# Performance work log

Hardware: AMD Instinct MI355X
Metric: run time of the kernel (lower is better)

The kernel has to match this reference:

```python
import jax, jax.numpy as jnp
import numpy as np

MOD = 26
N = 64  # module init arg n
B = 1024


def _mul_map():
    # A[p, k, v] = 1 where v = p*k mod MOD
    P_, K_ = np.meshgrid(np.arange(MOD), np.arange(MOD), indexing='ij')
    A = np.zeros((MOD, MOD, MOD), dtype=np.float32)
    A[P_, K_, (P_ * K_) % MOD] = 1.0
    return A


def _circ_conv(a, b):
    # circular convolution of length MOD via rfft/irfft, then clamp+normalize
    c = jnp.fft.irfft(jnp.fft.rfft(a, n=MOD) * jnp.fft.rfft(b, n=MOD), n=MOD)
    c = jnp.clip(c, 0.0)
    s = jnp.sum(c, axis=-1, keepdims=True)
    s = jnp.where(s == 0, jnp.ones_like(s), s)
    return c / s


def setup_inputs() -> dict:
    key = jax.random.key(0)
    k1, k2 = jax.random.split(key)
    P = jax.random.randint(k1, (B, N), 0, MOD)
    key_param = jax.random.normal(k2, (N * N, MOD), dtype=jnp.float32) * 0.01
    return {"P": P, "key_param": key_param}


def reference(P, key_param):
    n = N
    key_probs = jax.nn.softmax(key_param, axis=-1).reshape(n, n, MOD)
    A = jnp.asarray(_mul_map())  # [p, k, v]
    P_onehot = jax.nn.one_hot(P, MOD, dtype=jnp.float32)  # [B, n, MOD]
    # torch.tensordot(key_probs, A, dims=([2],[1])) -> [l, i, p, c]
    Kp_all = jnp.einsum('lik,pkc->lipc', key_probs, A)
    prod = jnp.einsum('blp,lipc->blic', P_onehot, Kp_all)  # [B, n_j, n_i, MOD]
    # sequential chain of circular convolutions over j, vectorized over (B, i)
    init = prod[:, 0]  # [B, n_i, MOD]
    xs = jnp.moveaxis(prod[:, 1:], 1, 0)  # [n-1, B, n_i, MOD]

    def step(dist, pj):
        return _circ_conv(dist, pj), None

    dist, _ = jax.lax.scan(step, init, xs)  # [B, n_i, MOD]
    log_probs = jnp.log(dist + 1e-12)
    return log_probs, key_probs
```

## Files before the change

kernel.cpp:

```cpp
#include <hip/hip_runtime.h>
#include <hip/hip_fp16.h>

#define MODV 26
#define HALFV 13
#define NV 64
#define BV 1024

typedef float v2f __attribute__((ext_vector_type(2)));
typedef _Float16 h2 __attribute__((ext_vector_type(2)));


__device__ __forceinline__ h2 bch2(uint u) { return __builtin_bit_cast(h2, u); }
__device__ __forceinline__ uint bcu(h2 v) { return __builtin_bit_cast(uint, v); }

__device__ __forceinline__ uint packw(v2f v)
{
    uint hs = (uint)__half_as_ushort(__float2half_rn(v.x));
    uint hd = (uint)__half_as_ushort(__float2half_rn(v.y));
    return hs | (hd << 16);
}

__device__ __forceinline__ void mulspec_w(h2* __restrict__ RE,
                                          h2* __restrict__ IM,
                                          const uint* __restrict__ w13)
{
    RE[0] *= bch2(w13[0]);
#pragma unroll
    for (int j = 1; j < 7; j++) {
        h2 kr = bch2(w13[j]), ki = bch2(w13[6 + j]);
        h2 nre = RE[j] * kr - IM[j] * ki;
        h2 nim = RE[j] * ki + IM[j] * kr;
        RE[j] = nre; IM[j] = nim;
    }
}

__global__ __launch_bounds__(256)
void prep_kernel(const float* __restrict__ key_param,
                 float* __restrict__ key_probs_out,
                 uint* __restrict__ ws)
{
    __shared__ float slab[NV * MODV];
    int l = blockIdx.x;
    int t = threadIdx.x;
    int i = t & 63;
    int w = t >> 6;
    int p = (blockIdx.y << 2) + w;

#pragma unroll
    for (int j = 0; j < 7; j++) {
        int idx = t + j * 256;
        if (idx < NV * MODV) slab[idx] = key_param[l * NV * MODV + idx];
    }
    __syncthreads();

    float x[MODV];
    float m = -1e30f;
#pragma unroll
    for (int k = 0; k < MODV; k++) {
        x[k] = slab[i * MODV + k];
        m = fmaxf(m, x[k]);
    }
    float s = 0.f;
#pragma unroll
    for (int k = 0; k < MODV; k++) { x[k] = __expf(x[k] - m); s += x[k]; }
    float inv = 1.f / s;
#pragma unroll
    for (int k = 0; k < MODV; k++) x[k] *= inv;

    if (blockIdx.y == 0 && w == 0) {
#pragma unroll
        for (int k = 0; k < MODV; k++)
            key_probs_out[((l << 6) + i) * MODV + k] = x[k];
    }
    if (p >= MODV) return;

    float c13[HALFV], s13[HALFV];
#pragma unroll
    for (int k = 0; k < HALFV; k++) {
        float a = 0.4833219467f * (float)k;
        __sincosf(a, &s13[k], &c13[k]);
    }

#pragma unroll
    for (int pc = 0; pc < MODV; pc++) {
        if (pc != p) continue;

        float Kp[MODV];
#pragma unroll
        for (int c = 0; c < MODV; c++) Kp[c] = 0.f;
#pragma unroll
        for (int k = 0; k < MODV; k++) Kp[(pc * k) % MODV] += x[k];

        v2f V[HALFV];
#pragma unroll
        for (int r = 0; r < HALFV; r++) {
            int c0 = (14 * r) % MODV;
            int c1 = (13 + 14 * r) % MODV;
            v2f v; v.x = Kp[c0] + Kp[c1]; v.y = Kp[c0] - Kp[c1];
            V[r] = v;
        }

        uint hw[HALFV];
        {
            v2f acc = V[0];
#pragma unroll
            for (int r = 1; r < HALFV; r++) acc += V[r];
            hw[0] = packw(acc);
        }
#pragma unroll
        for (int j = 1; j < 7; j++) {
            v2f re = V[0];
            v2f im; im.x = 0.f; im.y = 0.f;
#pragma unroll
            for (int r = 1; r < HALFV; r++) {
                int a = (j * r) % HALFV;
                re += V[r] * c13[a];
                im -= V[r] * s13[a];
            }
            hw[j]     = packw(re);
            hw[6 + j] = packw(im);
        }
        uint* dst = ws + ((size_t)(l * MODV + pc) << 10);
        *(uint4*)(dst + (i << 2))         = make_uint4(hw[0], hw[1], hw[2],  hw[3]);
        *(uint4*)(dst + 256 + (i << 2))   = make_uint4(hw[4], hw[5], hw[6],  hw[7]);
        *(uint4*)(dst + 512 + (i << 2))   = make_uint4(hw[8], hw[9], hw[10], hw[11]);
        dst[768 + i] = hw[12];
    }
}

__global__ __launch_bounds__(256, 4)
void chain_kernel(const int* __restrict__ P,
                  const uint* __restrict__ ws,
                  float* __restrict__ out)
{
    __shared__ int Pl[NV];
    __shared__ uint sbuf[2][64][HALFV];
    __shared__ float obuf[NV * MODV];

    int b = blockIdx.x;
    int w = threadIdx.x >> 6;
    int i = threadIdx.x & 63;
    if (threadIdx.x < NV) Pl[threadIdx.x] = P[(b << 6) + threadIdx.x];
    __syncthreads();

    int base = w << 4;
    int i4 = i << 2;

    h2 RE[7], IM[7];
    {
        const uint* e = ws + ((size_t)(base * MODV + Pl[base]) << 10);
        uint4 a  = *(const uint4*)(e + i4);
        uint4 bq = *(const uint4*)(e + 256 + i4);
        uint4 cq = *(const uint4*)(e + 512 + i4);
        uint w12 = e[768 + i];
        uint wd[HALFV] = {a.x, a.y, a.z, a.w, bq.x, bq.y, bq.z, bq.w,
                          cq.x, cq.y, cq.z, cq.w, w12};
#pragma unroll
        for (int j = 0; j < 7; j++) RE[j] = bch2(wd[j]);
#pragma unroll
        for (int j = 1; j < 7; j++) IM[j] = bch2(wd[6 + j]);
    }

    uint4 n0, n1, n2; uint n12;
    {
        int l = base + 1;
        const uint* e = ws + ((size_t)(l * MODV + Pl[l]) << 10);
        n0 = *(const uint4*)(e + i4);      n1 = *(const uint4*)(e + 256 + i4);
        n2 = *(const uint4*)(e + 512 + i4); n12 = e[768 + i];
    }

#pragma unroll 1
    for (int s = 1; s < 16; s++) {
        uint cw[HALFV] = {n0.x, n0.y, n0.z, n0.w, n1.x, n1.y, n1.z, n1.w,
                          n2.x, n2.y, n2.z, n2.w, n12};
        if (s < 15) {
            int l = base + s + 1;
            const uint* e = ws + ((size_t)(l * MODV + Pl[l]) << 10);
            n0 = *(const uint4*)(e + i4);      n1 = *(const uint4*)(e + 256 + i4);
            n2 = *(const uint4*)(e + 512 + i4); n12 = e[768 + i];
        }
        mulspec_w(RE, IM, cw);
    }

    if (w == 1 || w == 3) {
        int buf = w >> 1;
#pragma unroll
        for (int j = 0; j < 7; j++) sbuf[buf][i][j] = bcu(RE[j]);
#pragma unroll
        for (int j = 1; j < 7; j++) sbuf[buf][i][6 + j] = bcu(IM[j]);
    }
    __syncthreads();
    if (w == 0) {
        uint K[HALFV];
#pragma unroll
        for (int r = 0; r < HALFV; r++) K[r] = sbuf[0][i][r];
        mulspec_w(RE, IM, K);
    } else if (w == 2) {
        uint K[HALFV];
#pragma unroll
        for (int r = 0; r < HALFV; r++) K[r] = sbuf[1][i][r];
        mulspec_w(RE, IM, K);
#pragma unroll
        for (int j = 0; j < 7; j++) sbuf[1][i][j] = bcu(RE[j]);
#pragma unroll
        for (int j = 1; j < 7; j++) sbuf[1][i][6 + j] = bcu(IM[j]);
    }
    __syncthreads();
    if (w == 0) {
        uint K[HALFV];
#pragma unroll
        for (int r = 0; r < HALFV; r++) K[r] = sbuf[1][i][r];
        mulspec_w(RE, IM, K);

        v2f fRE[7], fIM[7];
#pragma unroll
        for (int j = 0; j < 7; j++) {
            v2f v; v.x = (float)RE[j].x; v.y = (float)RE[j].y; fRE[j] = v;
        }
#pragma unroll
        for (int j = 1; j < 7; j++) {
            v2f v; v.x = (float)IM[j].x; v.y = (float)IM[j].y; fIM[j] = v;
        }

        float c13[HALFV], s13[HALFV];
#pragma unroll
        for (int k = 0; k < HALFV; k++) {
            float a = 0.4833219467f * (float)k;
            __sincosf(a, &s13[k], &c13[k]);
        }
        v2f V[HALFV];
#pragma unroll
        for (int r = 0; r < HALFV; r++) {
            v2f acc = fRE[0];
#pragma unroll
            for (int j = 1; j < 7; j++) {
                int a = (j * r) % HALFV;
                acc += (fRE[j] * c13[a] - fIM[j] * s13[a]) * 2.0f;
            }
            V[r] = acc;
        }

        float tot = 0.f;
#pragma unroll
        for (int r = 0; r < HALFV; r++) tot += V[r].x;
        float invt = 0.5f / tot;

        float u[MODV];
#pragma unroll
        for (int r = 0; r < HALFV; r++) {
            u[(14 * r) % MODV]      = (V[r].x + V[r].y) * invt;
            u[(13 + 14 * r) % MODV] = (V[r].x - V[r].y) * invt;
        }
#pragma unroll
        for (int c = 0; c < MODV; c++)
            obuf[i * MODV + c] = __logf(u[c] + 1e-12f);
    }
    __syncthreads();

    {
        float* o = out + (size_t)b * (NV * MODV);
        int t = threadIdx.x;
#pragma unroll
        for (int k = 0; k < 6; k++)
            o[t + k * 256] = obuf[t + k * 256];
        int idx = t + 1536;
        if (idx < NV * MODV) o[idx] = obuf[idx];
    }
}

extern "C" void kernel_launch(void* const* d_in, const int* in_sizes, int n_in,
                              void* d_out, int out_size, void* d_ws, size_t ws_size,
                              hipStream_t stream)
{
    const int*   P  = (const int*)d_in[0];
    const float* kp = (const float*)d_in[1];
    float* out = (float*)d_out;
    float* key_probs_out = out + (size_t)BV * NV * MODV;
    uint* ws = (uint*)d_ws;

    hipLaunchKernelGGL(prep_kernel, dim3(64, 7), dim3(256), 0, stream,
                       kp, key_probs_out, ws);
    hipLaunchKernelGGL(chain_kernel, dim3(BV), dim3(256), 0, stream,
                       P, ws, out);
}
```

Before: 77.73 us.

## Spread final inverse DFT across all warps, deepen prefetch, compact workspace stride

The final inverse transform and log, which ran on one wavefront, is now split across all 256 threads: each thread handles a few output frequency pairs for one row, with twiddles read from a shared-memory table. The chain loop is unrolled by two with double-buffered prefetch of the next two spectra, so more loads are in flight. The workspace entry stride shrinks from 1024 to 832 words, making it denser in cache. The normaliser is now taken as 13 times the DC term instead of summing the reconstructed values, which is algebraically equivalent. The cost is an extra shared-memory round trip and one more barrier.

```diff
diff --git a/kernel.cpp b/kernel.cpp
--- a/kernel.cpp
+++ b/kernel.cpp
@@ -5,6 +5,7 @@
 #define HALFV 13
 #define NV 64
 #define BV 1024
+#define ESTRIDE 832
 
 typedef float v2f __attribute__((ext_vector_type(2)));
 typedef _Float16 h2 __attribute__((ext_vector_type(2)));
@@ -120,7 +121,7 @@
             hw[j]     = packw(re);
             hw[6 + j] = packw(im);
         }
-        uint* dst = ws + ((size_t)(l * MODV + pc) << 10);
+        uint* dst = ws + (size_t)(l * MODV + pc) * ESTRIDE;
         *(uint4*)(dst + (i << 2))         = make_uint4(hw[0], hw[1], hw[2],  hw[3]);
         *(uint4*)(dst + 256 + (i << 2))   = make_uint4(hw[4], hw[5], hw[6],  hw[7]);
         *(uint4*)(dst + 512 + (i << 2))   = make_uint4(hw[8], hw[9], hw[10], hw[11]);
@@ -136,23 +137,37 @@
     __shared__ int Pl[NV];
     __shared__ uint sbuf[2][64][HALFV];
     __shared__ float obuf[NV * MODV];
+    __shared__ float c2tab[HALFV], s2tab[HALFV];
 
     int b = blockIdx.x;
     int w = threadIdx.x >> 6;
     int i = threadIdx.x & 63;
     if (threadIdx.x < NV) Pl[threadIdx.x] = P[(b << 6) + threadIdx.x];
+    if (threadIdx.x < HALFV) {
+        float a = 0.4833219467f * (float)threadIdx.x;
+        float sv, cv;
+        __sincosf(a, &sv, &cv);
+        c2tab[threadIdx.x] = 2.f * cv;
+        s2tab[threadIdx.x] = 2.f * sv;
+    }
     __syncthreads();
 
     int base = w << 4;
     int i4 = i << 2;
 
+#define LOADE(v0, v1, v2, v12, l_)                                        \
+    {                                                                     \
+        const uint* e_ = ws + (size_t)((l_) * MODV + Pl[l_]) * ESTRIDE;   \
+        v0  = *(const uint4*)(e_ + i4);                                   \
+        v1  = *(const uint4*)(e_ + 256 + i4);                             \
+        v2  = *(const uint4*)(e_ + 512 + i4);                             \
+        v12 = e_[768 + i];                                                \
+    }
+
     h2 RE[7], IM[7];
     {
-        const uint* e = ws + ((size_t)(base * MODV + Pl[base]) << 10);
-        uint4 a  = *(const uint4*)(e + i4);
-        uint4 bq = *(const uint4*)(e + 256 + i4);
-        uint4 cq = *(const uint4*)(e + 512 + i4);
-        uint w12 = e[768 + i];
+        uint4 a, bq, cq; uint w12;
+        LOADE(a, bq, cq, w12, base);
         uint wd[HALFV] = {a.x, a.y, a.z, a.w, bq.x, bq.y, bq.z, bq.w,
                           cq.x, cq.y, cq.z, cq.w, w12};
 #pragma unroll
@@ -161,26 +176,31 @@
         for (int j = 1; j < 7; j++) IM[j] = bch2(wd[6 + j]);
     }
 
-    uint4 n0, n1, n2; uint n12;
+    uint4 A0, A1, A2, B0, B1, B2; uint A12, B12;
+    LOADE(A0, A1, A2, A12, base + 1);
+    LOADE(B0, B1, B2, B12, base + 2);
+
+#pragma unroll 1
+    for (int s = 1; s <= 13; s += 2) {
+        {
+            uint cw[HALFV] = {A0.x, A0.y, A0.z, A0.w, A1.x, A1.y, A1.z, A1.w,
+                              A2.x, A2.y, A2.z, A2.w, A12};
+            LOADE(A0, A1, A2, A12, base + s + 2);
+            mulspec_w(RE, IM, cw);
+        }
+        {
+            uint cw[HALFV] = {B0.x, B0.y, B0.z, B0.w, B1.x, B1.y, B1.z, B1.w,
+                              B2.x, B2.y, B2.z, B2.w, B12};
+            if (s + 3 <= 15) LOADE(B0, B1, B2, B12, base + s + 3);
+            mulspec_w(RE, IM, cw);
+        }
+    }
     {
-        int l = base + 1;
-        const uint* e = ws + ((size_t)(l * MODV + Pl[l]) << 10);
-        n0 = *(const uint4*)(e + i4);      n1 = *(const uint4*)(e + 256 + i4);
-        n2 = *(const uint4*)(e + 512 + i4); n12 = e[768 + i];
-    }
-
-#pragma unroll 1
-    for (int s = 1; s < 16; s++) {
-        uint cw[HALFV] = {n0.x, n0.y, n0.z, n0.w, n1.x, n1.y, n1.z, n1.w,
-                          n2.x, n2.y, n2.z, n2.w, n12};
-        if (s < 15) {
-            int l = base + s + 1;
-            const uint* e = ws + ((size_t)(l * MODV + Pl[l]) << 10);
-            n0 = *(const uint4*)(e + i4);      n1 = *(const uint4*)(e + 256 + i4);
-            n2 = *(const uint4*)(e + 512 + i4); n12 = e[768 + i];
-        }
+        uint cw[HALFV] = {A0.x, A0.y, A0.z, A0.w, A1.x, A1.y, A1.z, A1.w,
+                          A2.x, A2.y, A2.z, A2.w, A12};
         mulspec_w(RE, IM, cw);
     }
+#undef LOADE
 
     if (w == 1 || w == 3) {
         int buf = w >> 1;
@@ -211,49 +231,51 @@
 #pragma unroll
         for (int r = 0; r < HALFV; r++) K[r] = sbuf[1][i][r];
         mulspec_w(RE, IM, K);
-
-        v2f fRE[7], fIM[7];
+#pragma unroll
+        for (int j = 0; j < 7; j++) sbuf[0][i][j] = bcu(RE[j]);
+#pragma unroll
+        for (int j = 1; j < 7; j++) sbuf[0][i][6 + j] = bcu(IM[j]);
+    }
+    __syncthreads();
+
+    {
+        int ir = threadIdx.x >> 2;
+        int q  = threadIdx.x & 3;
+
+        uint wrow[HALFV];
+#pragma unroll
+        for (int j = 0; j < HALFV; j++) wrow[j] = sbuf[0][ir][j];
+
+        v2f fR[7], fI[7];
 #pragma unroll
         for (int j = 0; j < 7; j++) {
-            v2f v; v.x = (float)RE[j].x; v.y = (float)RE[j].y; fRE[j] = v;
+            h2 h = bch2(wrow[j]);
+            v2f v; v.x = (float)h.x; v.y = (float)h.y; fR[j] = v;
         }
 #pragma unroll
         for (int j = 1; j < 7; j++) {
-            v2f v; v.x = (float)IM[j].x; v.y = (float)IM[j].y; fIM[j] = v;
-        }
-
-        float c13[HALFV], s13[HALFV];
-#pragma unroll
-        for (int k = 0; k < HALFV; k++) {
-            float a = 0.4833219467f * (float)k;
-            __sincosf(a, &s13[k], &c13[k]);
-        }
-        v2f V[HALFV];
-#pragma unroll
-        for (int r = 0; r < HALFV; r++) {
-            v2f acc = fRE[0];
-#pragma unroll
-            for (int j = 1; j < 7; j++) {
-                int a = (j * r) % HALFV;
-                acc += (fRE[j] * c13[a] - fIM[j] * s13[a]) * 2.0f;
+            h2 h = bch2(wrow[6 + j]);
+            v2f v; v.x = (float)h.x; v.y = (float)h.y; fI[j] = v;
+        }
+        float invt = 0.5f / (13.0f * fR[0].x);
+
+#pragma unroll
+        for (int rr = 0; rr < 4; rr++) {
+            int r = q + (rr << 2);
+            if (r < HALFV) {
+                v2f acc = fR[0];
+                int a = 0;
+#pragma unroll
+                for (int j = 1; j < 7; j++) {
+                    a += r; if (a >= HALFV) a -= HALFV;
+                    acc += fR[j] * c2tab[a] - fI[j] * s2tab[a];
+                }
+                int c0 = (14 * r) % MODV;
+                int c1 = c0 + 13; if (c1 >= MODV) c1 -= MODV;
+                obuf[ir * MODV + c0] = __logf((acc.x + acc.y) * invt + 1e-12f);
+                obuf[ir * MODV + c1] = __logf((acc.x - acc.y) * invt + 1e-12f);
             }
-            V[r] = acc;
-        }
-
-        float tot = 0.f;
-#pragma unroll
-        for (int r = 0; r < HALFV; r++) tot += V[r].x;
-        float invt = 0.5f / tot;
-
-        float u[MODV];
-#pragma unroll
-        for (int r = 0; r < HALFV; r++) {
-            u[(14 * r) % MODV]      = (V[r].x + V[r].y) * invt;
-            u[(13 + 14 * r) % MODV] = (V[r].x - V[r].y) * invt;
-        }
-#pragma unroll
-        for (int c = 0; c < MODV; c++)
-            obuf[i * MODV + c] = __logf(u[c] + 1e-12f);
+        }
     }
     __syncthreads();
 
```

Measured after the change: 78.53 us. Within noise of the previous version (+1.0%).
